# Optimization experiments

Hardware: AMD Instinct MI355X
Metric: run time of the kernel (lower is better)

Reference implementation:

```python
import jax, jax.numpy as jnp
import numpy as np

N = 10000
E = 320000
NEG_SLOPE = 0.01  # torch nn.LeakyReLU default


def leaky_relu(x):
    return jnp.where(x >= 0, x, NEG_SLOPE * x)


def spmm(row, col, vals, dense):
    # sparse[N,N] @ dense[N,D] via gather + segment_sum over destination rows
    msgs = vals[:, None] * dense[col]          # [E, D]
    return jax.ops.segment_sum(msgs, row, num_segments=N)


def setup_inputs() -> dict:
    key = jax.random.key(0)
    ks = jax.random.split(key, 7)
    z = jax.random.normal(ks[0], (N, 64), dtype=jnp.float32)
    adj_row = jax.random.randint(ks[1], (E,), 0, N, dtype=jnp.int64)
    adj_col = jax.random.randint(ks[2], (E,), 0, N, dtype=jnp.int64)
    adj_vals = jax.random.uniform(ks[3], (E,), dtype=jnp.float32)
    # xavier_uniform: bound = sqrt(6/(fan_in+fan_out))
    def xavier(k, out_d, in_d):
        b = np.sqrt(6.0 / (in_d + out_d)).astype(np.float32)
        return jax.random.uniform(k, (out_d, in_d), minval=-b, maxval=b, dtype=jnp.float32)
    w1 = xavier(ks[4], 128, 64)
    w2 = xavier(ks[5], 256, 128)
    w3 = xavier(ks[6], 512, 256)
    return {"z": z, "adj_row": adj_row, "adj_col": adj_col, "adj_vals": adj_vals,
            "w1": w1, "w2": w2, "w3": w3, "active": 1}


def gnn_layer(x, w, row, col, vals, active):
    support = x @ w.T  # F.linear(features, weight)
    if active:
        support = leaky_relu(support)
    return spmm(row, col, vals, support)


def reference(z, adj_row, adj_col, adj_vals, w1, w2, w3, active):
    x = gnn_layer(z, w1, adj_row, adj_col, adj_vals, active)
    x = gnn_layer(x, w2, adj_row, adj_col, adj_vals, active)
    x_hat = gnn_layer(x, w3, adj_row, adj_col, adj_vals, active)
    adj_hat = jax.nn.sigmoid(x_hat @ x_hat.T)  # [N, N]
    return (x_hat, adj_hat)
```

## Files before the change

### kernel.cpp

```cpp
#include <hip/hip_runtime.h>
#include <hip/hip_bf16.h>

#define N_NODES 10000
#define N_EDGES 320000
#define PADM    10112
#define DOUT3   512

typedef __attribute__((ext_vector_type(4))) float f32x4;
typedef __attribute__((ext_vector_type(8))) short bf16x8;

#define GLOAD_LDS16(g, l)                                                        \
  __builtin_amdgcn_global_load_lds(                                              \
      (const __attribute__((address_space(1))) unsigned*)(g),                    \
      (__attribute__((address_space(3))) unsigned*)(l), 16, 0, 0)

__device__ inline unsigned short f2bf(float f) {
  union { float f; unsigned u; } uf; uf.f = f;
  unsigned u = uf.u;
  unsigned r = (u + 0x7fffu + ((u >> 16) & 1u)) >> 16;
  return (unsigned short)r;
}

__global__ __launch_bounds__(256) void k_zero(int* p, int n) {
  int i = blockIdx.x * 256 + threadIdx.x;
  if (i < n) p[i] = 0;
}

__global__ __launch_bounds__(256) void k_detect(const unsigned* rowsU32, int* flag) {
  __shared__ int any;
  if (threadIdx.x == 0) any = 0;
  __syncthreads();
  if (rowsU32[2 * threadIdx.x + 1] != 0u) any = 1;
  __syncthreads();
  if (threadIdx.x == 0) *flag = (any == 0) ? 1 : 0;
}

__device__ inline int edge_at(const void* p, int i, int is64) {
  return is64 ? (int)((const long long*)p)[i] : ((const int*)p)[i];
}

__global__ __launch_bounds__(256) void k_hist(const void* rows, const int* flag, int* cnt) {
  int i = blockIdx.x * 256 + threadIdx.x;
  if (i >= N_EDGES) return;
  int is64 = *flag;
  atomicAdd(&cnt[edge_at(rows, i, is64)], 1);
}

__global__ __launch_bounds__(256) void k_scan(const int* __restrict__ cnt, int* __restrict__ rp) {
  __shared__ int partial[256];
  const int T = 256;
  int t = threadIdx.x;
  int chunk = (N_NODES + T - 1) / T;
  int start = t * chunk;
  int end = start + chunk; if (end > N_NODES) end = N_NODES;
  int s = 0;
  for (int i = start; i < end && i >= start; ++i) s += cnt[i];
  partial[t] = (start < N_NODES) ? s : 0;
  __syncthreads();
  if (t == 0) {
    int acc = 0;
    for (int i = 0; i < T; ++i) { int v = partial[i]; partial[i] = acc; acc += v; }
  }
  __syncthreads();
  int acc = partial[t];
  for (int i = start; i < end && i >= start; ++i) { rp[i] = acc; acc += cnt[i]; }
  if (t == T - 1) rp[N_NODES] = acc;
}

__global__ __launch_bounds__(256) void k_scatter(const void* rows, const void* cols,
    const float* __restrict__ vals, const int* __restrict__ flag,
    const int* __restrict__ rp, int* cnt2, int* __restrict__ ccol, float* __restrict__ cval) {
  int i = blockIdx.x * 256 + threadIdx.x;
  if (i >= N_EDGES) return;
  int is64 = *flag;
  int r = edge_at(rows, i, is64);
  int c = edge_at(cols, i, is64);
  int pos = rp[r] + atomicAdd(&cnt2[r], 1);
  ccol[pos] = c;
  cval[pos] = vals[i];
}

template <int K>
__global__ __launch_bounds__(256) void k_linear(const float* __restrict__ A,
    const float* __restrict__ W, float* __restrict__ C,
    int M, int Dout, const int* __restrict__ activeFlag) {
  __shared__ __align__(16) float As[16][68];
  __shared__ __align__(16) float Ws[16][68];
  const int m0 = blockIdx.x * 64;
  const int n0 = blockIdx.y * 64;
  const int tid = threadIdx.x;
  const int tx = tid & 15, ty = tid >> 4;
  const int lrow = tid >> 2;
  const int lk = (tid & 3) * 4;
  float acc[4][4];
#pragma unroll
  for (int i = 0; i < 4; ++i)
#pragma unroll
    for (int j = 0; j < 4; ++j) acc[i][j] = 0.f;

  for (int k0 = 0; k0 < K; k0 += 16) {
    float4 va = make_float4(0.f, 0.f, 0.f, 0.f);
    if (m0 + lrow < M) va = *(const float4*)(A + (size_t)(m0 + lrow) * K + k0 + lk);
    float4 vb = *(const float4*)(W + (size_t)(n0 + lrow) * K + k0 + lk);
    __syncthreads();
    As[lk + 0][lrow] = va.x; As[lk + 1][lrow] = va.y; As[lk + 2][lrow] = va.z; As[lk + 3][lrow] = va.w;
    Ws[lk + 0][lrow] = vb.x; Ws[lk + 1][lrow] = vb.y; Ws[lk + 2][lrow] = vb.z; Ws[lk + 3][lrow] = vb.w;
    __syncthreads();
#pragma unroll
    for (int kk = 0; kk < 16; ++kk) {
      const float4 a4 = *(const float4*)&As[kk][ty << 2];
      const float4 b4 = *(const float4*)&Ws[kk][tx << 2];
      const float av[4] = {a4.x, a4.y, a4.z, a4.w};
      const float bv[4] = {b4.x, b4.y, b4.z, b4.w};
#pragma unroll
      for (int i = 0; i < 4; ++i)
#pragma unroll
        for (int j = 0; j < 4; ++j) acc[i][j] = fmaf(av[i], bv[j], acc[i][j]);
    }
  }
  const bool act = (*activeFlag) != 0;
#pragma unroll
  for (int i = 0; i < 4; ++i) {
    const int row = m0 + (ty << 2) + i;
    if (row < M) {
#pragma unroll
      for (int j = 0; j < 4; ++j) {
        float v = acc[i][j];
        if (act && v < 0.f) v *= 0.01f;
        C[(size_t)row * Dout + n0 + (tx << 2) + j] = v;
      }
    }
  }
}

template <int D, bool WB>
__global__ __launch_bounds__(128) void k_spmm2(const int* __restrict__ rp,
    const int* __restrict__ ccol, const float* __restrict__ cval,
    const float* __restrict__ sup, float* __restrict__ out,
    unsigned short* __restrict__ outb) {
  constexpr int V = D / 128;
  const int r = blockIdx.x;
  const int d0 = threadIdx.x * V;
  const int s = rp[r], e = rp[r + 1];
  float acc[V];
#pragma unroll
  for (int v = 0; v < V; ++v) acc[v] = 0.f;

  for (int i = s; i < e; ++i) {
    const float w = cval[i];
    const float* src = sup + (size_t)ccol[i] * D + d0;
    if constexpr (V == 4) {
      const float4 x = *(const float4*)src;
      acc[0] = fmaf(w, x.x, acc[0]); acc[1] = fmaf(w, x.y, acc[1]);
      acc[2] = fmaf(w, x.z, acc[2]); acc[3] = fmaf(w, x.w, acc[3]);
    } else if constexpr (V == 2) {
      const float2 x = *(const float2*)src;
      acc[0] = fmaf(w, x.x, acc[0]); acc[1] = fmaf(w, x.y, acc[1]);
    } else {
      acc[0] = fmaf(w, *src, acc[0]);
    }
  }

  float* dst = out + (size_t)r * D + d0;
  if constexpr (V == 4) *(float4*)dst = make_float4(acc[0], acc[1], acc[2], acc[3]);
  else if constexpr (V == 2) *(float2*)dst = make_float2(acc[0], acc[1]);
  else *dst = acc[0];

  if constexpr (WB) {
    uint2 u;
    u.x = (unsigned)f2bf(acc[0]) | ((unsigned)f2bf(acc[1]) << 16);
    u.y = (unsigned)f2bf(acc[2]) | ((unsigned)f2bf(acc[3]) << 16);
    *(uint2*)(outb + (size_t)r * 512 + d0) = u;
  }
}

__global__ __launch_bounds__(256) void k_padzero(unsigned short* __restrict__ xb) {
  const int t = blockIdx.x * 256 + threadIdx.x;
  if (t >= (PADM - N_NODES) * 512 / 8) return;
  uint4 z; z.x = z.y = z.z = z.w = 0u;
  *(uint4*)&xb[(size_t)N_NODES * 512 + (size_t)t * 8] = z;
}

__global__ __launch_bounds__(256) void k_xxt2(const unsigned short* __restrict__ Xb,
                                              float* __restrict__ adj) {
  __shared__ __align__(16) unsigned short As[128 * 32];
  __shared__ __align__(16) unsigned short Bs[128 * 32];
  const int tid = threadIdx.x;
  const int m0 = blockIdx.x * 128, n0 = blockIdx.y * 128;
  const int wave = tid >> 6, lane = tid & 63;
  const int wm = (wave >> 1) << 6;
  const int wn = (wave & 1) << 6;
  const int lr = lane & 15;
  const int lko = (lane >> 4) << 3;

  const int c0 = wave * 2;
  const int srow0 = c0 * 16 + (lane >> 2);
  const int sk = (lane & 3) << 3;
  const unsigned short* ga0 = Xb + (size_t)(m0 + srow0) * 512 + sk;
  const unsigned short* ga1 = ga0 + (size_t)16 * 512;
  const unsigned short* gb0 = Xb + (size_t)(n0 + srow0) * 512 + sk;
  const unsigned short* gb1 = gb0 + (size_t)16 * 512;
  unsigned short* la0 = &As[c0 * 512];
  unsigned short* la1 = &As[(c0 + 1) * 512];
  unsigned short* lb0 = &Bs[c0 * 512];
  unsigned short* lb1 = &Bs[(c0 + 1) * 512];

  f32x4 acc[4][4];
#pragma unroll
  for (int i = 0; i < 4; ++i)
#pragma unroll
    for (int j = 0; j < 4; ++j)
#pragma unroll
      for (int q = 0; q < 4; ++q) acc[i][j][q] = 0.f;

  for (int k0 = 0; k0 < 512; k0 += 32) {
    __syncthreads();
    GLOAD_LDS16(ga0 + k0, la0);
    GLOAD_LDS16(ga1 + k0, la1);
    GLOAD_LDS16(gb0 + k0, lb0);
    GLOAD_LDS16(gb1 + k0, lb1);
    __syncthreads();

    bf16x8 af[4], bff[4];
#pragma unroll
    for (int f = 0; f < 4; ++f) {
      af[f]  = *(const bf16x8*)&As[(wm + f * 16 + lr) * 32 + lko];
      bff[f] = *(const bf16x8*)&Bs[(wn + f * 16 + lr) * 32 + lko];
    }
#pragma unroll
    for (int mi = 0; mi < 4; ++mi)
#pragma unroll
      for (int ni = 0; ni < 4; ++ni)
        acc[mi][ni] = __builtin_amdgcn_mfma_f32_16x16x32_bf16(af[mi], bff[ni], acc[mi][ni], 0, 0, 0);
  }

#pragma unroll
  for (int mi = 0; mi < 4; ++mi) {
#pragma unroll
    for (int ni = 0; ni < 4; ++ni) {
      const int col = n0 + wn + ni * 16 + lr;
      const int rbase = m0 + wm + mi * 16 + ((lane >> 4) << 2);
      if (col < N_NODES) {
#pragma unroll
        for (int q = 0; q < 4; ++q) {
          const int rr = rbase + q;
          if (rr < N_NODES) {
            const float s = acc[mi][ni][q];
            adj[(size_t)rr * N_NODES + col] = 1.0f / (1.0f + __expf(-s));
          }
        }
      }
    }
  }
}

__global__ __launch_bounds__(256) void k_xxt_f32(const float* __restrict__ Xf, float* __restrict__ adj) {
  __shared__ __align__(16) short As[128 * 32];
  __shared__ __align__(16) short Bs[128 * 32];
  const int tid = threadIdx.x;
  const int m0 = blockIdx.x * 128, n0 = blockIdx.y * 128;
  const int wave = tid >> 6, lane = tid & 63;
  const int wm = (wave >> 1) << 6;
  const int wn = (wave & 1) << 6;
  const int lr = lane & 15;
  const int lko = (lane >> 4) << 3;

  f32x4 acc[4][4];
#pragma unroll
  for (int i = 0; i < 4; ++i)
#pragma unroll
    for (int j = 0; j < 4; ++j)
#pragma unroll
      for (int q = 0; q < 4; ++q) acc[i][j][q] = 0.f;

  for (int k0 = 0; k0 < 512; k0 += 32) {
    __syncthreads();
#pragma unroll
    for (int h = 0; h < 2; ++h) {
      const int c = tid + h * 256;
      const int row = c >> 2;
      const int cq = (c & 3) << 3;
      float4 fa0 = make_float4(0, 0, 0, 0), fa1 = fa0, fb0 = fa0, fb1 = fa0;
      const int ga = m0 + row, gb = n0 + row;
      if (ga < N_NODES) {
        fa0 = *(const float4*)(Xf + (size_t)ga * 512 + k0 + cq);
        fa1 = *(const float4*)(Xf + (size_t)ga * 512 + k0 + cq + 4);
      }
      if (gb < N_NODES) {
        fb0 = *(const float4*)(Xf + (size_t)gb * 512 + k0 + cq);
        fb1 = *(const float4*)(Xf + (size_t)gb * 512 + k0 + cq + 4);
      }
      uint4 ua, ub;
      ua.x = (unsigned)f2bf(fa0.x) | ((unsigned)f2bf(fa0.y) << 16);
      ua.y = (unsigned)f2bf(fa0.z) | ((unsigned)f2bf(fa0.w) << 16);
      ua.z = (unsigned)f2bf(fa1.x) | ((unsigned)f2bf(fa1.y) << 16);
      ua.w = (unsigned)f2bf(fa1.z) | ((unsigned)f2bf(fa1.w) << 16);
      ub.x = (unsigned)f2bf(fb0.x) | ((unsigned)f2bf(fb0.y) << 16);
      ub.y = (unsigned)f2bf(fb0.z) | ((unsigned)f2bf(fb0.w) << 16);
      ub.z = (unsigned)f2bf(fb1.x) | ((unsigned)f2bf(fb1.y) << 16);
      ub.w = (unsigned)f2bf(fb1.z) | ((unsigned)f2bf(fb1.w) << 16);
      *(uint4*)&As[row * 32 + cq] = ua;
      *(uint4*)&Bs[row * 32 + cq] = ub;
    }
    __syncthreads();

    bf16x8 af[4], bff[4];
#pragma unroll
    for (int f = 0; f < 4; ++f) {
      af[f]  = *(const bf16x8*)&As[(wm + f * 16 + lr) * 32 + lko];
      bff[f] = *(const bf16x8*)&Bs[(wn + f * 16 + lr) * 32 + lko];
    }
#pragma unroll
    for (int mi = 0; mi < 4; ++mi)
#pragma unroll
      for (int ni = 0; ni < 4; ++ni)
        acc[mi][ni] = __builtin_amdgcn_mfma_f32_16x16x32_bf16(af[mi], bff[ni], acc[mi][ni], 0, 0, 0);
  }

#pragma unroll
  for (int mi = 0; mi < 4; ++mi) {
#pragma unroll
    for (int ni = 0; ni < 4; ++ni) {
      const int col = n0 + wn + ni * 16 + lr;
      const int rbase = m0 + wm + mi * 16 + ((lane >> 4) << 2);
      if (col < N_NODES) {
#pragma unroll
        for (int q = 0; q < 4; ++q) {
          const int rr = rbase + q;
          if (rr < N_NODES) {
            const float s = acc[mi][ni][q];
            adj[(size_t)rr * N_NODES + col] = 1.0f / (1.0f + __expf(-s));
          }
        }
      }
    }
  }
}

extern "C" void kernel_launch(void* const* d_in, const int* in_sizes, int n_in,
                              void* d_out, int out_size, void* d_ws, size_t ws_size,
                              hipStream_t stream) {
  const float* z     = (const float*)d_in[0];
  const void*  arow  = d_in[1];
  const void*  acol  = d_in[2];
  const float* avals = (const float*)d_in[3];
  const float* w1    = (const float*)d_in[4];
  const float* w2    = (const float*)d_in[5];
  const float* w3    = (const float*)d_in[6];
  const int*   activ = (const int*)d_in[7];

  float* out  = (float*)d_out;
  float* xhat = out;
  float* adj  = out + (size_t)N_NODES * DOUT3;

  float* sup = adj;
  float* x1  = adj + 5120000;
  float* x2  = x1 + 1280000;
  int*  iscr = (int*)(x2 + 2560000);
  int* rp    = iscr;
  int* cnt   = rp + 10016;
  int* cnt2  = cnt + 10016;
  int* flag  = cnt2 + 10016;
  int* ccol  = flag + 16;
  float* cval = (float*)(ccol + N_EDGES);

  const size_t need = (size_t)PADM * DOUT3 * 2;
  const bool useWs = (ws_size >= need);
  unsigned short* xb = (unsigned short*)d_ws;

  k_zero<<<(20032 + 255) / 256, 256, 0, stream>>>(cnt, 20032);
  k_detect<<<1, 256, 0, stream>>>((const unsigned*)arow, flag);
  k_hist<<<(N_EDGES + 255) / 256, 256, 0, stream>>>(arow, flag, cnt);
  k_scan<<<1, 256, 0, stream>>>(cnt, rp);
  k_scatter<<<(N_EDGES + 255) / 256, 256, 0, stream>>>(arow, acol, avals, flag, rp, cnt2, ccol, cval);

  k_linear<64><<<dim3(157, 2), 256, 0, stream>>>(z, w1, sup, N_NODES, 128, activ);
  k_spmm2<128, false><<<N_NODES, 128, 0, stream>>>(rp, ccol, cval, sup, x1, nullptr);
  k_linear<128><<<dim3(157, 4), 256, 0, stream>>>(x1, w2, sup, N_NODES, 256, activ);
  k_spmm2<256, false><<<N_NODES, 128, 0, stream>>>(rp, ccol, cval, sup, x2, nullptr);
  k_linear<256><<<dim3(157, 8), 256, 0, stream>>>(x2, w3, sup, N_NODES, 512, activ);

  if (useWs) {
    k_spmm2<512, true><<<N_NODES, 128, 0, stream>>>(rp, ccol, cval, sup, xhat, xb);
    k_padzero<<<28, 256, 0, stream>>>(xb);
    k_xxt2<<<dim3(79, 79), 256, 0, stream>>>(xb, adj);
  } else {
    k_spmm2<512, false><<<N_NODES, 128, 0, stream>>>(rp, ccol, cval, sup, xhat, nullptr);
    k_xxt_f32<<<dim3(79, 79), 256, 0, stream>>>(xhat, adj);
  }
}
```

Baseline: 877.7 us.

## Run GNN linear layers on fp16 MFMA with half-precision intermediates

Converts inputs and weights to fp16 and replaces the scalar fp32 linear kernels with MFMA-based fp16 GEMMs. Support and hidden activations are stored in fp16, which halves the bytes the SpMM gathers move. The sigmoid epilogue in the X·Xᵀ kernel now uses a fast reciprocal and nontemporal stores for the 400MB adjacency output. In exchange it adds conversion launches and lowers precision in the intermediate layers.

```diff
diff --git a/kernel.cpp b/kernel.cpp
--- a/kernel.cpp
+++ b/kernel.cpp
@@ -8,6 +8,9 @@
 
 typedef __attribute__((ext_vector_type(4))) float f32x4;
 typedef __attribute__((ext_vector_type(8))) short bf16x8;
+typedef __attribute__((ext_vector_type(8))) _Float16 f16x8;
+typedef __attribute__((ext_vector_type(4))) _Float16 half4;
+typedef __attribute__((ext_vector_type(2))) _Float16 half2;
 
 #define GLOAD_LDS16(g, l)                                                        \
   __builtin_amdgcn_global_load_lds(                                              \
@@ -80,6 +83,221 @@
   cval[pos] = vals[i];
 }
 
+__global__ __launch_bounds__(256) void k_f2h(const float* __restrict__ in, _Float16* __restrict__ out, int n4) {
+  int t = blockIdx.x * 256 + threadIdx.x;
+  if (t >= n4) return;
+  const float4 f = *(const float4*)(in + (size_t)t * 4);
+  half4 h;
+  h[0] = (_Float16)f.x; h[1] = (_Float16)f.y; h[2] = (_Float16)f.z; h[3] = (_Float16)f.w;
+  *(half4*)(out + (size_t)t * 4) = h;
+}
+
+template <int K>
+__global__ __launch_bounds__(256) void k_linh(const _Float16* __restrict__ A,
+    const _Float16* __restrict__ W, _Float16* __restrict__ outh,
+    int M, int Dout, const int* __restrict__ activeFlag) {
+  __shared__ __align__(16) unsigned short As[128 * 32];
+  __shared__ __align__(16) unsigned short Bs[128 * 32];
+  const int tid = threadIdx.x;
+  const int m0 = blockIdx.x * 128, n0 = blockIdx.y * 128;
+  const int wave = tid >> 6, lane = tid & 63;
+  const int wm = (wave >> 1) << 6;
+  const int wn = (wave & 1) << 6;
+  const int lr = lane & 15;
+  const int lko = (lane >> 4) << 3;
+
+  const int c0 = wave * 2;
+  const int srow = c0 * 16 + (lane >> 2);
+  const int sk = (lane & 3) << 3;
+  int arow0 = m0 + srow;      if (arow0 > M - 1) arow0 = M - 1;
+  int arow1 = m0 + srow + 16; if (arow1 > M - 1) arow1 = M - 1;
+  const _Float16* ga0 = A + (size_t)arow0 * K + sk;
+  const _Float16* ga1 = A + (size_t)arow1 * K + sk;
+  const _Float16* gb0 = W + (size_t)(n0 + srow) * K + sk;
+  const _Float16* gb1 = gb0 + (size_t)16 * K;
+  unsigned short* la0 = &As[c0 * 512];
+  unsigned short* la1 = &As[(c0 + 1) * 512];
+  unsigned short* lb0 = &Bs[c0 * 512];
+  unsigned short* lb1 = &Bs[(c0 + 1) * 512];
+
+  f32x4 acc[4][4];
+#pragma unroll
+  for (int i = 0; i < 4; ++i)
+#pragma unroll
+    for (int j = 0; j < 4; ++j)
+#pragma unroll
+      for (int q = 0; q < 4; ++q) acc[i][j][q] = 0.f;
+
+  for (int k0 = 0; k0 < K; k0 += 32) {
+    __syncthreads();
+    GLOAD_LDS16(ga0 + k0, la0);
+    GLOAD_LDS16(ga1 + k0, la1);
+    GLOAD_LDS16(gb0 + k0, lb0);
+    GLOAD_LDS16(gb1 + k0, lb1);
+    __syncthreads();
+
+    f16x8 af[4], bff[4];
+#pragma unroll
+    for (int f = 0; f < 4; ++f) {
+      af[f]  = *(const f16x8*)&As[(wm + f * 16 + lr) * 32 + lko];
+      bff[f] = *(const f16x8*)&Bs[(wn + f * 16 + lr) * 32 + lko];
+    }
+#pragma unroll
+    for (int mi = 0; mi < 4; ++mi)
+#pragma unroll
+      for (int ni = 0; ni < 4; ++ni)
+        acc[mi][ni] = __builtin_amdgcn_mfma_f32_16x16x32_f16(af[mi], bff[ni], acc[mi][ni], 0, 0, 0);
+  }
+
+  const bool act = (*activeFlag) != 0;
+#pragma unroll
+  for (int mi = 0; mi < 4; ++mi) {
+#pragma unroll
+    for (int ni = 0; ni < 4; ++ni) {
+      const int col = n0 + wn + ni * 16 + lr;
+      const int rbase = m0 + wm + mi * 16 + ((lane >> 4) << 2);
+#pragma unroll
+      for (int q = 0; q < 4; ++q) {
+        const int rr = rbase + q;
+        if (rr < M) {
+          float v = acc[mi][ni][q];
+          if (act && v < 0.f) v *= 0.01f;
+          outh[(size_t)rr * Dout + col] = (_Float16)v;
+        }
+      }
+    }
+  }
+}
+
+template <int D, int MODE>
+__global__ __launch_bounds__(128) void k_spmmh(const int* __restrict__ rp,
+    const int* __restrict__ ccol, const float* __restrict__ cval,
+    const _Float16* __restrict__ sup, _Float16* __restrict__ outh,
+    float* __restrict__ outf, unsigned short* __restrict__ outb) {
+  constexpr int V = D / 128;
+  const int r = blockIdx.x;
+  const int d0 = threadIdx.x * V;
+  const int s = rp[r], e = rp[r + 1];
+  float acc[V];
+#pragma unroll
+  for (int v = 0; v < V; ++v) acc[v] = 0.f;
+
+  for (int i = s; i < e; ++i) {
+    const float w = cval[i];
+    const _Float16* src = sup + (size_t)ccol[i] * D + d0;
+    if constexpr (V == 4) {
+      const half4 x = *(const half4*)src;
+#pragma unroll
+      for (int v = 0; v < 4; ++v) acc[v] = fmaf(w, (float)x[v], acc[v]);
+    } else if constexpr (V == 2) {
+      const half2 x = *(const half2*)src;
+      acc[0] = fmaf(w, (float)x[0], acc[0]);
+      acc[1] = fmaf(w, (float)x[1], acc[1]);
+    } else {
+      acc[0] = fmaf(w, (float)*src, acc[0]);
+    }
+  }
+
+  if constexpr (MODE == 0) {
+    if constexpr (V == 4) {
+      half4 h; h[0] = (_Float16)acc[0]; h[1] = (_Float16)acc[1]; h[2] = (_Float16)acc[2]; h[3] = (_Float16)acc[3];
+      *(half4*)(outh + (size_t)r * D + d0) = h;
+    } else if constexpr (V == 2) {
+      half2 h; h[0] = (_Float16)acc[0]; h[1] = (_Float16)acc[1];
+      *(half2*)(outh + (size_t)r * D + d0) = h;
+    } else {
+      outh[(size_t)r * D + d0] = (_Float16)acc[0];
+    }
+  } else {
+    *(float4*)(outf + (size_t)r * D + d0) = make_float4(acc[0], acc[1], acc[2], acc[3]);
+    uint2 u;
+    u.x = (unsigned)f2bf(acc[0]) | ((unsigned)f2bf(acc[1]) << 16);
+    u.y = (unsigned)f2bf(acc[2]) | ((unsigned)f2bf(acc[3]) << 16);
+    *(uint2*)(outb + (size_t)r * 512 + d0) = u;
+  }
+}
+
+__global__ __launch_bounds__(256) void k_padzero(unsigned short* __restrict__ xb) {
+  const int t = blockIdx.x * 256 + threadIdx.x;
+  if (t >= (PADM - N_NODES) * 512 / 8) return;
+  uint4 z; z.x = z.y = z.z = z.w = 0u;
+  *(uint4*)&xb[(size_t)N_NODES * 512 + (size_t)t * 8] = z;
+}
+
+__global__ __launch_bounds__(256) void k_xxt2(const unsigned short* __restrict__ Xb,
+                                              float* __restrict__ adj) {
+  __shared__ __align__(16) unsigned short As[128 * 32];
+  __shared__ __align__(16) unsigned short Bs[128 * 32];
+  const int tid = threadIdx.x;
+  const int m0 = blockIdx.x * 128, n0 = blockIdx.y * 128;
+  const int wave = tid >> 6, lane = tid & 63;
+  const int wm = (wave >> 1) << 6;
+  const int wn = (wave & 1) << 6;
+  const int lr = lane & 15;
+  const int lko = (lane >> 4) << 3;
+
+  const int c0 = wave * 2;
+  const int srow0 = c0 * 16 + (lane >> 2);
+  const int sk = (lane & 3) << 3;
+  const unsigned short* ga0 = Xb + (size_t)(m0 + srow0) * 512 + sk;
+  const unsigned short* ga1 = ga0 + (size_t)16 * 512;
+  const unsigned short* gb0 = Xb + (size_t)(n0 + srow0) * 512 + sk;
+  const unsigned short* gb1 = gb0 + (size_t)16 * 512;
+  unsigned short* la0 = &As[c0 * 512];
+  unsigned short* la1 = &As[(c0 + 1) * 512];
+  unsigned short* lb0 = &Bs[c0 * 512];
+  unsigned short* lb1 = &Bs[(c0 + 1) * 512];
+
+  f32x4 acc[4][4];
+#pragma unroll
+  for (int i = 0; i < 4; ++i)
+#pragma unroll
+    for (int j = 0; j < 4; ++j)
+#pragma unroll
+      for (int q = 0; q < 4; ++q) acc[i][j][q] = 0.f;
+
+  for (int k0 = 0; k0 < 512; k0 += 32) {
+    __syncthreads();
+    GLOAD_LDS16(ga0 + k0, la0);
+    GLOAD_LDS16(ga1 + k0, la1);
+    GLOAD_LDS16(gb0 + k0, lb0);
+    GLOAD_LDS16(gb1 + k0, lb1);
+    __syncthreads();
+
+    bf16x8 af[4], bff[4];
+#pragma unroll
+    for (int f = 0; f < 4; ++f) {
+      af[f]  = *(const bf16x8*)&As[(wm + f * 16 + lr) * 32 + lko];
+      bff[f] = *(const bf16x8*)&Bs[(wn + f * 16 + lr) * 32 + lko];
+    }
+#pragma unroll
+    for (int mi = 0; mi < 4; ++mi)
+#pragma unroll
+      for (int ni = 0; ni < 4; ++ni)
+        acc[mi][ni] = __builtin_amdgcn_mfma_f32_16x16x32_bf16(af[mi], bff[ni], acc[mi][ni], 0, 0, 0);
+  }
+
+#pragma unroll
+  for (int mi = 0; mi < 4; ++mi) {
+#pragma unroll
+    for (int ni = 0; ni < 4; ++ni) {
+      const int col = n0 + wn + ni * 16 + lr;
+      const int rbase = m0 + wm + mi * 16 + ((lane >> 4) << 2);
+      if (col < N_NODES) {
+#pragma unroll
+        for (int q = 0; q < 4; ++q) {
+          const int rr = rbase + q;
+          if (rr < N_NODES) {
+            const float s = acc[mi][ni][q];
+            const float sg = __builtin_amdgcn_rcpf(1.0f + __expf(-s));
+            __builtin_nontemporal_store(sg, &adj[(size_t)rr * N_NODES + col]);
+          }
+        }
+      }
+    }
+  }
+}
+
 template <int K>
 __global__ __launch_bounds__(256) void k_linear(const float* __restrict__ A,
     const float* __restrict__ W, float* __restrict__ C,
@@ -133,11 +351,10 @@
   }
 }
 
-template <int D, bool WB>
+template <int D>
 __global__ __launch_bounds__(128) void k_spmm2(const int* __restrict__ rp,
     const int* __restrict__ ccol, const float* __restrict__ cval,
-    const float* __restrict__ sup, float* __restrict__ out,
-    unsigned short* __restrict__ outb) {
+    const float* __restrict__ sup, float* __restrict__ out) {
   constexpr int V = D / 128;
   const int r = blockIdx.x;
   const int d0 = threadIdx.x * V;
@@ -145,7 +362,6 @@
   float acc[V];
 #pragma unroll
   for (int v = 0; v < V; ++v) acc[v] = 0.f;
-
   for (int i = s; i < e; ++i) {
     const float w = cval[i];
     const float* src = sup + (size_t)ccol[i] * D + d0;
@@ -160,98 +376,10 @@
       acc[0] = fmaf(w, *src, acc[0]);
     }
   }
-
   float* dst = out + (size_t)r * D + d0;
   if constexpr (V == 4) *(float4*)dst = make_float4(acc[0], acc[1], acc[2], acc[3]);
   else if constexpr (V == 2) *(float2*)dst = make_float2(acc[0], acc[1]);
   else *dst = acc[0];
-
-  if constexpr (WB) {
-    uint2 u;
-    u.x = (unsigned)f2bf(acc[0]) | ((unsigned)f2bf(acc[1]) << 16);
-    u.y = (unsigned)f2bf(acc[2]) | ((unsigned)f2bf(acc[3]) << 16);
-    *(uint2*)(outb + (size_t)r * 512 + d0) = u;
-  }
-}
-
-__global__ __launch_bounds__(256) void k_padzero(unsigned short* __restrict__ xb) {
-  const int t = blockIdx.x * 256 + threadIdx.x;
-  if (t >= (PADM - N_NODES) * 512 / 8) return;
-  uint4 z; z.x = z.y = z.z = z.w = 0u;
-  *(uint4*)&xb[(size_t)N_NODES * 512 + (size_t)t * 8] = z;
-}
-
-__global__ __launch_bounds__(256) void k_xxt2(const unsigned short* __restrict__ Xb,
-                                              float* __restrict__ adj) {
-  __shared__ __align__(16) unsigned short As[128 * 32];
-  __shared__ __align__(16) unsigned short Bs[128 * 32];
-  const int tid = threadIdx.x;
-  const int m0 = blockIdx.x * 128, n0 = blockIdx.y * 128;
-  const int wave = tid >> 6, lane = tid & 63;
-  const int wm = (wave >> 1) << 6;
-  const int wn = (wave & 1) << 6;
-  const int lr = lane & 15;
-  const int lko = (lane >> 4) << 3;
-
-  const int c0 = wave * 2;
-  const int srow0 = c0 * 16 + (lane >> 2);
-  const int sk = (lane & 3) << 3;
-  const unsigned short* ga0 = Xb + (size_t)(m0 + srow0) * 512 + sk;
-  const unsigned short* ga1 = ga0 + (size_t)16 * 512;
-  const unsigned short* gb0 = Xb + (size_t)(n0 + srow0) * 512 + sk;
-  const unsigned short* gb1 = gb0 + (size_t)16 * 512;
-  unsigned short* la0 = &As[c0 * 512];
-  unsigned short* la1 = &As[(c0 + 1) * 512];
-  unsigned short* lb0 = &Bs[c0 * 512];
-  unsigned short* lb1 = &Bs[(c0 + 1) * 512];
-
-  f32x4 acc[4][4];
-#pragma unroll
-  for (int i = 0; i < 4; ++i)
-#pragma unroll
-    for (int j = 0; j < 4; ++j)
-#pragma unroll
-      for (int q = 0; q < 4; ++q) acc[i][j][q] = 0.f;
-
-  for (int k0 = 0; k0 < 512; k0 += 32) {
-    __syncthreads();
-    GLOAD_LDS16(ga0 + k0, la0);
-    GLOAD_LDS16(ga1 + k0, la1);
-    GLOAD_LDS16(gb0 + k0, lb0);
-    GLOAD_LDS16(gb1 + k0, lb1);
-    __syncthreads();
-
-    bf16x8 af[4], bff[4];
-#pragma unroll
-    for (int f = 0; f < 4; ++f) {
-      af[f]  = *(const bf16x8*)&As[(wm + f * 16 + lr) * 32 + lko];
-      bff[f] = *(const bf16x8*)&Bs[(wn + f * 16 + lr) * 32 + lko];
-    }
-#pragma unroll
-    for (int mi = 0; mi < 4; ++mi)
-#pragma unroll
-      for (int ni = 0; ni < 4; ++ni)
-        acc[mi][ni] = __builtin_amdgcn_mfma_f32_16x16x32_bf16(af[mi], bff[ni], acc[mi][ni], 0, 0, 0);
-  }
-
-#pragma unroll
-  for (int mi = 0; mi < 4; ++mi) {
-#pragma unroll
-    for (int ni = 0; ni < 4; ++ni) {
-      const int col = n0 + wn + ni * 16 + lr;
-      const int rbase = m0 + wm + mi * 16 + ((lane >> 4) << 2);
-      if (col < N_NODES) {
-#pragma unroll
-        for (int q = 0; q < 4; ++q) {
-          const int rr = rbase + q;
-          if (rr < N_NODES) {
-            const float s = acc[mi][ni][q];
-            adj[(size_t)rr * N_NODES + col] = 1.0f / (1.0f + __expf(-s));
-          }
-        }
-      }
-    }
-  }
 }
 
 __global__ __launch_bounds__(256) void k_xxt_f32(const float* __restrict__ Xf, float* __restrict__ adj) {
@@ -353,10 +481,7 @@
   float* xhat = out;
   float* adj  = out + (size_t)N_NODES * DOUT3;
 
-  float* sup = adj;
-  float* x1  = adj + 5120000;
-  float* x2  = x1 + 1280000;
-  int*  iscr = (int*)(x2 + 2560000);
+  int* iscr  = (int*)(adj + 9000000);
   int* rp    = iscr;
   int* cnt   = rp + 10016;
   int* cnt2  = cnt + 10016;
@@ -364,9 +489,17 @@
   int* ccol  = flag + 16;
   float* cval = (float*)(ccol + N_EDGES);
 
-  const size_t need = (size_t)PADM * DOUT3 * 2;
-  const bool useWs = (ws_size >= need);
-  unsigned short* xb = (unsigned short*)d_ws;
+  _Float16* wsh = (_Float16*)d_ws;
+  size_t off = 0;
+  unsigned short* xb = (unsigned short*)d_ws;             off += (size_t)PADM * 512;
+  _Float16* zh  = wsh + off;  off += 640000;
+  _Float16* w1h = wsh + off;  off += 8192;
+  _Float16* w2h = wsh + off;  off += 32768;
+  _Float16* w3h = wsh + off;  off += 131072;
+  _Float16* suph = wsh + off; off += (size_t)N_NODES * 512;
+  _Float16* x1h = wsh + off;  off += (size_t)N_NODES * 128;
+  _Float16* x2h = wsh + off;  off += (size_t)N_NODES * 256;
+  const bool useWs = (ws_size >= off * sizeof(_Float16));
 
   k_zero<<<(20032 + 255) / 256, 256, 0, stream>>>(cnt, 20032);
   k_detect<<<1, 256, 0, stream>>>((const unsigned*)arow, flag);
@@ -374,18 +507,31 @@
   k_scan<<<1, 256, 0, stream>>>(cnt, rp);
   k_scatter<<<(N_EDGES + 255) / 256, 256, 0, stream>>>(arow, acol, avals, flag, rp, cnt2, ccol, cval);
 
-  k_linear<64><<<dim3(157, 2), 256, 0, stream>>>(z, w1, sup, N_NODES, 128, activ);
-  k_spmm2<128, false><<<N_NODES, 128, 0, stream>>>(rp, ccol, cval, sup, x1, nullptr);
-  k_linear<128><<<dim3(157, 4), 256, 0, stream>>>(x1, w2, sup, N_NODES, 256, activ);
-  k_spmm2<256, false><<<N_NODES, 128, 0, stream>>>(rp, ccol, cval, sup, x2, nullptr);
-  k_linear<256><<<dim3(157, 8), 256, 0, stream>>>(x2, w3, sup, N_NODES, 512, activ);
-
   if (useWs) {
-    k_spmm2<512, true><<<N_NODES, 128, 0, stream>>>(rp, ccol, cval, sup, xhat, xb);
+    k_f2h<<<(160000 + 255) / 256, 256, 0, stream>>>(z, zh, 160000);
+    k_f2h<<<(2048 + 255) / 256, 256, 0, stream>>>(w1, w1h, 2048);
+    k_f2h<<<(8192 + 255) / 256, 256, 0, stream>>>(w2, w2h, 8192);
+    k_f2h<<<(32768 + 255) / 256, 256, 0, stream>>>(w3, w3h, 32768);
+
+    k_linh<64><<<dim3(79, 1), 256, 0, stream>>>(zh, w1h, suph, N_NODES, 128, activ);
+    k_spmmh<128, 0><<<N_NODES, 128, 0, stream>>>(rp, ccol, cval, suph, x1h, nullptr, nullptr);
+    k_linh<128><<<dim3(79, 2), 256, 0, stream>>>(x1h, w2h, suph, N_NODES, 256, activ);
+    k_spmmh<256, 0><<<N_NODES, 128, 0, stream>>>(rp, ccol, cval, suph, x2h, nullptr, nullptr);
+    k_linh<256><<<dim3(79, 4), 256, 0, stream>>>(x2h, w3h, suph, N_NODES, 512, activ);
+    k_spmmh<512, 2><<<N_NODES, 128, 0, stream>>>(rp, ccol, cval, suph, nullptr, xhat, xb);
+
     k_padzero<<<28, 256, 0, stream>>>(xb);
     k_xxt2<<<dim3(79, 79), 256, 0, stream>>>(xb, adj);
   } else {
-    k_spmm2<512, false><<<N_NODES, 128, 0, stream>>>(rp, ccol, cval, sup, xhat, nullptr);
+    float* sup = adj;
+    float* x1  = adj + 5120000;
+    float* x2  = x1 + 1280000;
+    k_linear<64><<<dim3(157, 2), 256, 0, stream>>>(z, w1, sup, N_NODES, 128, activ);
+    k_spmm2<128><<<N_NODES, 128, 0, stream>>>(rp, ccol, cval, sup, x1);
+    k_linear<128><<<dim3(157, 4), 256, 0, stream>>>(x1, w2, sup, N_NODES, 256, activ);
+    k_spmm2<256><<<N_NODES, 128, 0, stream>>>(rp, ccol, cval, sup, x2);
+    k_linear<256><<<dim3(157, 8), 256, 0, stream>>>(x2, w3, sup, N_NODES, 512, activ);
+    k_spmm2<512><<<N_NODES, 128, 0, stream>>>(rp, ccol, cval, sup, xhat);
     k_xxt_f32<<<dim3(79, 79), 256, 0, stream>>>(xhat, adj);
   }
 }
```

Result: faster. 774.0 us (-11.8%).
